# Optimization experiments

Hardware: AMD Instinct MI355X
Metric: run time of the kernel (lower is better)

## Reference

```python
import jax, jax.numpy as jnp
import numpy as np

B, C, H, W = 16, 64, 64, 64
K = 1024  # n_embedding


def setup_inputs() -> dict:
    key = jax.random.key(0)
    k1, k2 = jax.random.split(key)
    x = jax.random.normal(k1, (B, C, H, W), dtype=jnp.float32)
    embedding = jax.random.normal(k2, (K, C), dtype=jnp.float32)
    return {"x": x, "embedding": embedding}


def reference(x, embedding):
    b, c, h, w = x.shape
    # [B,C,H,W] -> [N, C] tokens
    xf = jnp.transpose(x, (0, 2, 3, 1)).reshape(-1, c)
    # squared Euclidean distances (argmin-equivalent to torch.cdist p=2)
    d2 = (jnp.sum(xf * xf, axis=1, keepdims=True)
          - 2.0 * xf @ embedding.T
          + jnp.sum(embedding * embedding, axis=1)[None, :])  # [N, K]
    idx = jnp.argmin(d2, axis=-1)  # [N]
    q = embedding[idx]             # gather: [N, C]
    commitment_loss = jnp.mean((jax.lax.stop_gradient(q) - xf) ** 2)
    codebook_loss = jnp.mean((q - jax.lax.stop_gradient(xf)) ** 2)
    # straight-through estimator
    out = xf + jax.lax.stop_gradient(q - xf)
    x_q = jnp.transpose(out.reshape(b, h, w, c), (0, 3, 1, 2))
    indices = idx.reshape(-1, h, w)
    return x_q, codebook_loss, commitment_loss, indices
```

## Files before the change

### kernel.cpp

```cpp
#include <hip/hip_runtime.h>

typedef short s16x8 __attribute__((ext_vector_type(8)));
typedef float f32x4 __attribute__((ext_vector_type(4)));

#define CCH 64
#define KCB 1024
#define HWSZ 4096
#define CHW 262144
#define NXQ 4194304
#define NMEAN 4194304.0
#define PLANE_BYTES 131072

static __device__ __forceinline__ unsigned short f2bf(float f) {
    unsigned int u = __float_as_uint(f);
    return (unsigned short)((u + 0x7FFFu + ((u >> 16) & 1u)) >> 16);
}
static __device__ __forceinline__ float bf2f(unsigned short b) {
    return __uint_as_float(((unsigned int)b) << 16);
}

__global__ void vq_prep(const float* __restrict__ E, float* __restrict__ e2,
                        s16x8* __restrict__ Bh, s16x8* __restrict__ Bm,
                        s16x8* __restrict__ Bl, double* __restrict__ loss_acc) {
    int gid = blockIdx.x * blockDim.x + threadIdx.x;
    if (gid == 0) *loss_acc = 0.0;
    {
        int nt = gid >> 7, rem = gid & 127;
        int ks = rem >> 6, l = rem & 63;
        int code = nt * 16 + (l & 15);
        int cb   = ks * 32 + ((l >> 4) << 3);
        const float* ep = E + code * CCH + cb;
        s16x8 vh, vm, vl;
#pragma unroll
        for (int j = 0; j < 8; ++j) {
            float v = -2.f * ep[j];
            unsigned short h  = f2bf(v);  float r1 = v  - bf2f(h);
            unsigned short md = f2bf(r1); float r2 = r1 - bf2f(md);
            unsigned short lo = f2bf(r2);
            vh[j] = (short)h; vm[j] = (short)md; vl[j] = (short)lo;
        }
        Bh[gid] = vh; Bm[gid] = vm; Bl[gid] = vl;
    }
    if (gid < KCB) {
        const float4* e4 = reinterpret_cast<const float4*>(E + gid * CCH);
        float s = 0.f;
#pragma unroll
        for (int i = 0; i < 16; ++i) {
            float4 v = e4[i];
            s = fmaf(v.x, v.x, s); s = fmaf(v.y, v.y, s);
            s = fmaf(v.z, v.z, s); s = fmaf(v.w, v.w, s);
        }
        e2[gid] = s;
    }
}

__global__ __launch_bounds__(256, 2) void vq_main(
    const float* __restrict__ x, const float* __restrict__ E,
    const s16x8* __restrict__ Bh, const s16x8* __restrict__ Bm,
    const s16x8* __restrict__ Bl, const float* __restrict__ e2,
    float* __restrict__ out, double* __restrict__ loss_acc)
{
    __shared__ s16x8 BB[2][768];
    __shared__ float BVL[128];
    __shared__ int   BIL[128];
    __shared__ float XSL[128];

    const int t    = threadIdx.x;
    const int lane = t & 63;
    const int w    = t >> 6;
    const int g    = lane >> 4;
    const int c15  = lane & 15;
    const int n0   = blockIdx.x * 128;
    const int b    = n0 >> 12;
    const int hw0  = n0 & 4095;

    s16x8 ah[2][2], am[2][2], al[2][2];
#pragma unroll
    for (int mt = 0; mt < 2; ++mt) {
        const float* xp = x + b * CHW + hw0 + w * 32 + mt * 16 + c15;
        float xs = 0.f;
#pragma unroll
        for (int ks = 0; ks < 2; ++ks)
#pragma unroll
            for (int j = 0; j < 8; ++j) {
                float v = xp[(ks * 32 + g * 8 + j) * HWSZ];
                xs = fmaf(v, v, xs);
                unsigned short h  = f2bf(v);  float r1 = v  - bf2f(h);
                unsigned short md = f2bf(r1); float r2 = r1 - bf2f(md);
                unsigned short lo = f2bf(r2);
                ah[mt][ks][j] = (short)h; am[mt][ks][j] = (short)md; al[mt][ks][j] = (short)lo;
            }
        xs += __shfl_xor(xs, 16, 64);
        xs += __shfl_xor(xs, 32, 64);
        if (lane < 16) XSL[w * 32 + mt * 16 + lane] = xs;
    }

    BB[0][t] = Bh[t]; BB[0][256 + t] = Bm[t]; BB[0][512 + t] = Bl[t];
    __syncthreads();

    float best[2][4]; int bidx[2][4];
#pragma unroll
    for (int mt = 0; mt < 2; ++mt)
#pragma unroll
        for (int r = 0; r < 4; ++r) { best[mt][r] = 3.4e38f; bidx[mt][r] = 0; }

    int buf = 0;
#pragma unroll 1
    for (int ch = 0; ch < 32; ++ch) {
        s16x8 sH, sM, sL;
        const int nb = (ch + 1) * 256 + t;
        if (ch < 31) { sH = Bh[nb]; sM = Bm[nb]; sL = Bl[nb]; }

#pragma unroll
        for (int nt = 0; nt < 2; ++nt) {
            const float s0 = e2[ch * 32 + nt * 16 + c15];
            s16x8 bh[2], bm[2], bl[2];
#pragma unroll
            for (int ks = 0; ks < 2; ++ks) {
                const int q = (nt * 2 + ks) * 64 + lane;
                bh[ks] = BB[buf][q];
                bm[ks] = BB[buf][256 + q];
                bl[ks] = BB[buf][512 + q];
            }
#pragma unroll
            for (int mt = 0; mt < 2; ++mt) {
                f32x4 acc = (f32x4){s0, s0, s0, s0};
#pragma unroll
                for (int ks = 0; ks < 2; ++ks) {
                    acc = __builtin_amdgcn_mfma_f32_16x16x32_bf16(ah[mt][ks], bh[ks], acc, 0, 0, 0);
                    acc = __builtin_amdgcn_mfma_f32_16x16x32_bf16(ah[mt][ks], bm[ks], acc, 0, 0, 0);
                    acc = __builtin_amdgcn_mfma_f32_16x16x32_bf16(am[mt][ks], bh[ks], acc, 0, 0, 0);
                    acc = __builtin_amdgcn_mfma_f32_16x16x32_bf16(am[mt][ks], bm[ks], acc, 0, 0, 0);
                    acc = __builtin_amdgcn_mfma_f32_16x16x32_bf16(ah[mt][ks], bl[ks], acc, 0, 0, 0);
                    acc = __builtin_amdgcn_mfma_f32_16x16x32_bf16(al[mt][ks], bh[ks], acc, 0, 0, 0);
                }
                const int k = ch * 32 + nt * 16 + c15;
#pragma unroll
                for (int r = 0; r < 4; ++r) {
                    float s = acc[r];
                    if (s < best[mt][r]) { best[mt][r] = s; bidx[mt][r] = k; }
                }
            }
        }

        if (ch < 31) {
            BB[buf ^ 1][t] = sH; BB[buf ^ 1][256 + t] = sM; BB[buf ^ 1][512 + t] = sL;
        }
        __syncthreads();
        buf ^= 1;
    }

#pragma unroll
    for (int mt = 0; mt < 2; ++mt)
#pragma unroll
        for (int r = 0; r < 4; ++r) {
            float v = best[mt][r]; int k = bidx[mt][r];
#pragma unroll
            for (int off = 1; off < 16; off <<= 1) {
                float ov = __shfl_xor(v, off, 64);
                int   ok = __shfl_xor(k, off, 64);
                if (ov < v || (ov == v && ok < k)) { v = ov; k = ok; }
            }
            if (c15 == 0) {
                BVL[w * 32 + mt * 16 + g * 4 + r] = v;
                BIL[w * 32 + mt * 16 + g * 4 + r] = k;
            }
        }
    __syncthreads();

    {
        const int tok = (w & 1) * 64 + lane;
        const int bi  = BIL[tok];
        const int cq  = w >> 1;
        const float4* eq = reinterpret_cast<const float4*>(E + bi * CCH + cq * 32);
        float* oq = out + b * CHW + (cq * 32) * HWSZ + hw0 + tok;
#pragma unroll
        for (int i = 0; i < 8; ++i) {
            float4 q = eq[i];
            oq[(4 * i + 0) * HWSZ] = q.x;
            oq[(4 * i + 1) * HWSZ] = q.y;
            oq[(4 * i + 2) * HWSZ] = q.z;
            oq[(4 * i + 3) * HWSZ] = q.w;
        }
        if (cq == 0) {
            out[NXQ + 2 + n0 + tok] = (float)bi;
            float lsum = BVL[tok] + XSL[tok];
#pragma unroll
            for (int off = 32; off > 0; off >>= 1)
                lsum += __shfl_xor(lsum, off, 64);
            if (lane == 0) atomicAdd(loss_acc, (double)lsum);
        }
    }
}

__global__ void vq_final(const double* __restrict__ loss_acc,
                         float* __restrict__ out) {
    if (threadIdx.x == 0) {
        float m = (float)(*loss_acc / NMEAN);
        out[NXQ]     = m;
        out[NXQ + 1] = m;
    }
}

extern "C" void kernel_launch(void* const* d_in, const int* in_sizes, int n_in,
                              void* d_out, int out_size, void* d_ws, size_t ws_size,
                              hipStream_t stream) {
    const float* x = (const float*)d_in[0];
    const float* E = (const float*)d_in[1];
    float* out = (float*)d_out;
    double* loss_acc = (double*)d_ws;
    float*  e2 = (float*)((char*)d_ws + 64);
    s16x8*  Bh = (s16x8*)((char*)d_ws + 8192);
    s16x8*  Bm = (s16x8*)((char*)d_ws + 8192 + PLANE_BYTES);
    s16x8*  Bl = (s16x8*)((char*)d_ws + 8192 + 2 * PLANE_BYTES);

    vq_prep <<<128, 64,  0, stream>>>(E, e2, Bh, Bm, Bl, loss_acc);
    vq_main <<<512, 256, 0, stream>>>(x, E, Bh, Bm, Bl, e2, out, loss_acc);
    vq_final<<<1,   64,  0, stream>>>(loss_acc, out);
}
```

Baseline: 128.3 us.

## Switch to fp16 hi/lo split with scaled residual and single-wave blocks

Replaces the three-way bf16 split (six MFMAs per k-step) with a two-way fp16 split whose low part is scaled by 2048, so each k-step needs three f16 MFMAs into two accumulators that are combined afterwards. The block shrinks to one wave of 64 tokens with four M-tiles. Codebook fragments are now read straight from global memory into registers with a register double buffer, which removes the LDS staging and the per-chunk barriers. This lowers MFMA count and synchronisation, but accuracy now depends on fp16 range and precision, which could flip argmin ties, and each wave does its own global codebook reads.

```diff
diff --git a/kernel.cpp b/kernel.cpp
--- a/kernel.cpp
+++ b/kernel.cpp
@@ -1,6 +1,6 @@
 #include <hip/hip_runtime.h>
 
-typedef short s16x8 __attribute__((ext_vector_type(8)));
+typedef _Float16 f16x8 __attribute__((ext_vector_type(8)));
 typedef float f32x4 __attribute__((ext_vector_type(4)));
 
 #define CCH 64
@@ -10,18 +10,11 @@
 #define NXQ 4194304
 #define NMEAN 4194304.0
 #define PLANE_BYTES 131072
-
-static __device__ __forceinline__ unsigned short f2bf(float f) {
-    unsigned int u = __float_as_uint(f);
-    return (unsigned short)((u + 0x7FFFu + ((u >> 16) & 1u)) >> 16);
-}
-static __device__ __forceinline__ float bf2f(unsigned short b) {
-    return __uint_as_float(((unsigned int)b) << 16);
-}
+#define INV2048 0.00048828125f
 
 __global__ void vq_prep(const float* __restrict__ E, float* __restrict__ e2,
-                        s16x8* __restrict__ Bh, s16x8* __restrict__ Bm,
-                        s16x8* __restrict__ Bl, double* __restrict__ loss_acc) {
+                        f16x8* __restrict__ Bh, f16x8* __restrict__ Bl,
+                        double* __restrict__ loss_acc) {
     int gid = blockIdx.x * blockDim.x + threadIdx.x;
     if (gid == 0) *loss_acc = 0.0;
     {
@@ -30,16 +23,16 @@
         int code = nt * 16 + (l & 15);
         int cb   = ks * 32 + ((l >> 4) << 3);
         const float* ep = E + code * CCH + cb;
-        s16x8 vh, vm, vl;
+        f16x8 vh, vl;
 #pragma unroll
         for (int j = 0; j < 8; ++j) {
             float v = -2.f * ep[j];
-            unsigned short h  = f2bf(v);  float r1 = v  - bf2f(h);
-            unsigned short md = f2bf(r1); float r2 = r1 - bf2f(md);
-            unsigned short lo = f2bf(r2);
-            vh[j] = (short)h; vm[j] = (short)md; vl[j] = (short)lo;
-        }
-        Bh[gid] = vh; Bm[gid] = vm; Bl[gid] = vl;
+            _Float16 h = (_Float16)v;
+            float r = v - (float)h;
+            vh[j] = h;
+            vl[j] = (_Float16)(r * 2048.0f);
+        }
+        Bh[gid] = vh; Bl[gid] = vl;
     }
     if (gid < KCB) {
         const float4* e4 = reinterpret_cast<const float4*>(E + gid * CCH);
@@ -54,30 +47,27 @@
     }
 }
 
-__global__ __launch_bounds__(256, 2) void vq_main(
+__global__ __launch_bounds__(64, 2) void vq_main(
     const float* __restrict__ x, const float* __restrict__ E,
-    const s16x8* __restrict__ Bh, const s16x8* __restrict__ Bm,
-    const s16x8* __restrict__ Bl, const float* __restrict__ e2,
-    float* __restrict__ out, double* __restrict__ loss_acc)
+    const f16x8* __restrict__ Bh, const f16x8* __restrict__ Bl,
+    const float* __restrict__ e2, float* __restrict__ out,
+    double* __restrict__ loss_acc)
 {
-    __shared__ s16x8 BB[2][768];
-    __shared__ float BVL[128];
-    __shared__ int   BIL[128];
-    __shared__ float XSL[128];
-
-    const int t    = threadIdx.x;
-    const int lane = t & 63;
-    const int w    = t >> 6;
+    __shared__ float XSL[64];
+    __shared__ float BVL[64];
+    __shared__ int   BIL[64];
+
+    const int lane = threadIdx.x;
     const int g    = lane >> 4;
     const int c15  = lane & 15;
-    const int n0   = blockIdx.x * 128;
+    const int n0   = blockIdx.x * 64;
     const int b    = n0 >> 12;
     const int hw0  = n0 & 4095;
 
-    s16x8 ah[2][2], am[2][2], al[2][2];
-#pragma unroll
-    for (int mt = 0; mt < 2; ++mt) {
-        const float* xp = x + b * CHW + hw0 + w * 32 + mt * 16 + c15;
+    f16x8 ah[4][2], al[4][2];
+#pragma unroll
+    for (int mt = 0; mt < 4; ++mt) {
+        const float* xp = x + b * CHW + hw0 + mt * 16 + c15;
         float xs = 0.f;
 #pragma unroll
         for (int ks = 0; ks < 2; ++ks)
@@ -85,73 +75,81 @@
             for (int j = 0; j < 8; ++j) {
                 float v = xp[(ks * 32 + g * 8 + j) * HWSZ];
                 xs = fmaf(v, v, xs);
-                unsigned short h  = f2bf(v);  float r1 = v  - bf2f(h);
-                unsigned short md = f2bf(r1); float r2 = r1 - bf2f(md);
-                unsigned short lo = f2bf(r2);
-                ah[mt][ks][j] = (short)h; am[mt][ks][j] = (short)md; al[mt][ks][j] = (short)lo;
+                _Float16 h = (_Float16)v;
+                float r = v - (float)h;
+                ah[mt][ks][j] = h;
+                al[mt][ks][j] = (_Float16)(r * 2048.0f);
             }
         xs += __shfl_xor(xs, 16, 64);
         xs += __shfl_xor(xs, 32, 64);
-        if (lane < 16) XSL[w * 32 + mt * 16 + lane] = xs;
-    }
-
-    BB[0][t] = Bh[t]; BB[0][256 + t] = Bm[t]; BB[0][512 + t] = Bl[t];
-    __syncthreads();
-
-    float best[2][4]; int bidx[2][4];
-#pragma unroll
-    for (int mt = 0; mt < 2; ++mt)
+        if (lane < 16) XSL[mt * 16 + lane] = xs;
+    }
+
+    float best[4][4]; int bidx[4][4];
+#pragma unroll
+    for (int mt = 0; mt < 4; ++mt)
 #pragma unroll
         for (int r = 0; r < 4; ++r) { best[mt][r] = 3.4e38f; bidx[mt][r] = 0; }
 
-    int buf = 0;
+    f16x8 cbh[2][2], cbl[2][2];
+#pragma unroll
+    for (int nt = 0; nt < 2; ++nt)
+#pragma unroll
+        for (int ks = 0; ks < 2; ++ks) {
+            int idx = (nt * 2 + ks) * 64 + lane;
+            cbh[nt][ks] = Bh[idx];
+            cbl[nt][ks] = Bl[idx];
+        }
+
 #pragma unroll 1
     for (int ch = 0; ch < 32; ++ch) {
-        s16x8 sH, sM, sL;
-        const int nb = (ch + 1) * 256 + t;
-        if (ch < 31) { sH = Bh[nb]; sM = Bm[nb]; sL = Bl[nb]; }
+        f16x8 nbh[2][2], nbl[2][2];
+        if (ch < 31) {
+#pragma unroll
+            for (int nt = 0; nt < 2; ++nt)
+#pragma unroll
+                for (int ks = 0; ks < 2; ++ks) {
+                    int idx = (((ch + 1) * 2 + nt) * 2 + ks) * 64 + lane;
+                    nbh[nt][ks] = Bh[idx];
+                    nbl[nt][ks] = Bl[idx];
+                }
+        }
 
 #pragma unroll
         for (int nt = 0; nt < 2; ++nt) {
             const float s0 = e2[ch * 32 + nt * 16 + c15];
-            s16x8 bh[2], bm[2], bl[2];
-#pragma unroll
-            for (int ks = 0; ks < 2; ++ks) {
-                const int q = (nt * 2 + ks) * 64 + lane;
-                bh[ks] = BB[buf][q];
-                bm[ks] = BB[buf][256 + q];
-                bl[ks] = BB[buf][512 + q];
-            }
-#pragma unroll
-            for (int mt = 0; mt < 2; ++mt) {
-                f32x4 acc = (f32x4){s0, s0, s0, s0};
+            const int k = ch * 32 + nt * 16 + c15;
+#pragma unroll
+            for (int mt = 0; mt < 4; ++mt) {
+                f32x4 a0 = (f32x4){s0, s0, s0, s0};
+                f32x4 a1 = (f32x4){0.f, 0.f, 0.f, 0.f};
 #pragma unroll
                 for (int ks = 0; ks < 2; ++ks) {
-                    acc = __builtin_amdgcn_mfma_f32_16x16x32_bf16(ah[mt][ks], bh[ks], acc, 0, 0, 0);
-                    acc = __builtin_amdgcn_mfma_f32_16x16x32_bf16(ah[mt][ks], bm[ks], acc, 0, 0, 0);
-                    acc = __builtin_amdgcn_mfma_f32_16x16x32_bf16(am[mt][ks], bh[ks], acc, 0, 0, 0);
-                    acc = __builtin_amdgcn_mfma_f32_16x16x32_bf16(am[mt][ks], bm[ks], acc, 0, 0, 0);
-                    acc = __builtin_amdgcn_mfma_f32_16x16x32_bf16(ah[mt][ks], bl[ks], acc, 0, 0, 0);
-                    acc = __builtin_amdgcn_mfma_f32_16x16x32_bf16(al[mt][ks], bh[ks], acc, 0, 0, 0);
-                }
-                const int k = ch * 32 + nt * 16 + c15;
+                    a0 = __builtin_amdgcn_mfma_f32_16x16x32_f16(ah[mt][ks], cbh[nt][ks], a0, 0, 0, 0);
+                    a1 = __builtin_amdgcn_mfma_f32_16x16x32_f16(ah[mt][ks], cbl[nt][ks], a1, 0, 0, 0);
+                    a1 = __builtin_amdgcn_mfma_f32_16x16x32_f16(al[mt][ks], cbh[nt][ks], a1, 0, 0, 0);
+                }
 #pragma unroll
                 for (int r = 0; r < 4; ++r) {
-                    float s = acc[r];
+                    float s = fmaf(a1[r], INV2048, a0[r]);
                     if (s < best[mt][r]) { best[mt][r] = s; bidx[mt][r] = k; }
                 }
             }
         }
 
         if (ch < 31) {
-            BB[buf ^ 1][t] = sH; BB[buf ^ 1][256 + t] = sM; BB[buf ^ 1][512 + t] = sL;
-        }
-        __syncthreads();
-        buf ^= 1;
-    }
-
-#pragma unroll
-    for (int mt = 0; mt < 2; ++mt)
+#pragma unroll
+            for (int nt = 0; nt < 2; ++nt)
+#pragma unroll
+                for (int ks = 0; ks < 2; ++ks) {
+                    cbh[nt][ks] = nbh[nt][ks];
+                    cbl[nt][ks] = nbl[nt][ks];
+                }
+        }
+    }
+
+#pragma unroll
+    for (int mt = 0; mt < 4; ++mt)
 #pragma unroll
         for (int r = 0; r < 4; ++r) {
             float v = best[mt][r]; int k = bidx[mt][r];
@@ -162,33 +160,35 @@
                 if (ov < v || (ov == v && ok < k)) { v = ov; k = ok; }
             }
             if (c15 == 0) {
-                BVL[w * 32 + mt * 16 + g * 4 + r] = v;
-                BIL[w * 32 + mt * 16 + g * 4 + r] = k;
+                BVL[mt * 16 + g * 4 + r] = v;
+                BIL[mt * 16 + g * 4 + r] = k;
             }
         }
     __syncthreads();
 
     {
-        const int tok = (w & 1) * 64 + lane;
-        const int bi  = BIL[tok];
-        const int cq  = w >> 1;
-        const float4* eq = reinterpret_cast<const float4*>(E + bi * CCH + cq * 32);
-        float* oq = out + b * CHW + (cq * 32) * HWSZ + hw0 + tok;
-#pragma unroll
-        for (int i = 0; i < 8; ++i) {
-            float4 q = eq[i];
-            oq[(4 * i + 0) * HWSZ] = q.x;
-            oq[(4 * i + 1) * HWSZ] = q.y;
-            oq[(4 * i + 2) * HWSZ] = q.z;
-            oq[(4 * i + 3) * HWSZ] = q.w;
-        }
-        if (cq == 0) {
-            out[NXQ + 2 + n0 + tok] = (float)bi;
-            float lsum = BVL[tok] + XSL[tok];
-#pragma unroll
-            for (int off = 32; off > 0; off >>= 1)
-                lsum += __shfl_xor(lsum, off, 64);
-            if (lane == 0) atomicAdd(loss_acc, (double)lsum);
+        const int bi = BIL[lane];
+        out[NXQ + 2 + n0 + lane] = (float)bi;
+
+        float lsum = BVL[lane] + XSL[lane];
+#pragma unroll
+        for (int off = 32; off > 0; off >>= 1)
+            lsum += __shfl_xor(lsum, off, 64);
+        if (lane == 0) atomicAdd(loss_acc, (double)lsum);
+
+        const float4* eq = reinterpret_cast<const float4*>(E + bi * CCH);
+        float* oq = out + b * CHW + hw0 + lane;
+#pragma unroll 1
+        for (int gq = 0; gq < 4; ++gq) {
+            float4 q0 = eq[4 * gq + 0];
+            float4 q1 = eq[4 * gq + 1];
+            float4 q2 = eq[4 * gq + 2];
+            float4 q3 = eq[4 * gq + 3];
+            float* o = oq + (16 * gq) * HWSZ;
+            o[0 * HWSZ]  = q0.x; o[1 * HWSZ]  = q0.y; o[2 * HWSZ]  = q0.z; o[3 * HWSZ]  = q0.w;
+            o[4 * HWSZ]  = q1.x; o[5 * HWSZ]  = q1.y; o[6 * HWSZ]  = q1.z; o[7 * HWSZ]  = q1.w;
+            o[8 * HWSZ]  = q2.x; o[9 * HWSZ]  = q2.y; o[10 * HWSZ] = q2.z; o[11 * HWSZ] = q2.w;
+            o[12 * HWSZ] = q3.x; o[13 * HWSZ] = q3.y; o[14 * HWSZ] = q3.z; o[15 * HWSZ] = q3.w;
         }
     }
 }
@@ -210,11 +210,10 @@
     float* out = (float*)d_out;
     double* loss_acc = (double*)d_ws;
     float*  e2 = (float*)((char*)d_ws + 64);
-    s16x8*  Bh = (s16x8*)((char*)d_ws + 8192);
-    s16x8*  Bm = (s16x8*)((char*)d_ws + 8192 + PLANE_BYTES);
-    s16x8*  Bl = (s16x8*)((char*)d_ws + 8192 + 2 * PLANE_BYTES);
-
-    vq_prep <<<128, 64,  0, stream>>>(E, e2, Bh, Bm, Bl, loss_acc);
-    vq_main <<<512, 256, 0, stream>>>(x, E, Bh, Bm, Bl, e2, out, loss_acc);
-    vq_final<<<1,   64,  0, stream>>>(loss_acc, out);
-}
+    f16x8*  Bh = (f16x8*)((char*)d_ws + 8192);
+    f16x8*  Bl = (f16x8*)((char*)d_ws + 8192 + PLANE_BYTES);
+
+    vq_prep <<<128,  64, 0, stream>>>(E, e2, Bh, Bl, loss_acc);
+    vq_main <<<1024, 64, 0, stream>>>(x, E, Bh, Bl, e2, out, loss_acc);
+    vq_final<<<1,    64, 0, stream>>>(loss_acc, out);
+}
```

After: 126.3 us. Within noise of the previous version (-1.5%).
